# Kernel tuning notes

Hardware: AMD Instinct MI355X
Metric: run time of the kernel (lower is better)

Reference implementation:

```python
import jax, jax.numpy as jnp
import numpy as np

B, L, D_MODEL = 4, 2048, 512
N_HEAD, D_K, D_V = 8, 64, 64
RANK = 20


def tt_linear(x, g1, g2, g3, g4, b):
    # TT-matrix linear: input modes (4,4,8,4), output modes (4,4,8,4), ranks [1,20,20,20,1]
    Bx, Lx, _ = x.shape
    t = x.reshape(Bx * Lx, 4, 4, 8, 4)
    t = jnp.einsum('bwxyz,wou->bxyzou', t, g1[0])        # g1: [1,m1,n1,r1]
    t = jnp.einsum('bxyzou,uxpv->byzopv', t, g2)         # g2: [r1,m2,n2,r2]
    t = jnp.einsum('byzopv,vyqw->bzopqw', t, g3)         # g3: [r2,m3,n3,r3]
    t = jnp.einsum('bzopqw,wzs->bopqs', t, g4[..., 0])   # g4: [r3,m4,n4,1]
    return t.reshape(Bx, Lx, -1) + b


def setup_inputs() -> dict:
    key = jax.random.key(0)
    ks = jax.random.split(key, 8)
    scale = jnp.float32(0.15)
    inp = {}
    for name, kk in zip(['wq', 'wk', 'wv', 'fc'], ks[:4]):
        sub = jax.random.split(kk, 4)
        inp[name + '_g1'] = jax.random.normal(sub[0], (1, 4, 4, RANK), jnp.float32) * scale
        inp[name + '_g2'] = jax.random.normal(sub[1], (RANK, 4, 4, RANK), jnp.float32) * scale
        inp[name + '_g3'] = jax.random.normal(sub[2], (RANK, 8, 8, RANK), jnp.float32) * scale
        inp[name + '_g4'] = jax.random.normal(sub[3], (RANK, 4, 4, 1), jnp.float32) * scale
        inp[name + '_b'] = jnp.zeros((D_MODEL,), jnp.float32)
    inp['q'] = jax.random.normal(ks[4], (B, L, D_MODEL), jnp.float32)
    inp['k'] = jax.random.normal(ks[5], (B, L, D_MODEL), jnp.float32)
    inp['v'] = jax.random.normal(ks[6], (B, L, D_MODEL), jnp.float32)
    inp['ln_g'] = jnp.ones((D_MODEL,), jnp.float32)
    inp['ln_b'] = jnp.zeros((D_MODEL,), jnp.float32)
    return inp


def reference(q, k, v,
              wq_g1, wq_g2, wq_g3, wq_g4, wq_b,
              wk_g1, wk_g2, wk_g3, wk_g4, wk_b,
              wv_g1, wv_g2, wv_g3, wv_g4, wv_b,
              fc_g1, fc_g2, fc_g3, fc_g4, fc_b,
              ln_g, ln_b):
    Bx, Lq, _ = q.shape
    residual = q
    qh = tt_linear(q, wq_g1, wq_g2, wq_g3, wq_g4, wq_b).reshape(Bx, Lq, N_HEAD, D_K).transpose(0, 2, 1, 3)
    kh = tt_linear(k, wk_g1, wk_g2, wk_g3, wk_g4, wk_b).reshape(Bx, Lq, N_HEAD, D_K).transpose(0, 2, 1, 3)
    vh = tt_linear(v, wv_g1, wv_g2, wv_g3, wv_g4, wv_b).reshape(Bx, Lq, N_HEAD, D_V).transpose(0, 2, 1, 3)
    temp = jnp.sqrt(jnp.float32(D_K))
    attn = jnp.einsum('bhqd,bhkd->bhqk', qh / temp, kh)  # explicit [B,H,L,L] scores
    attn = jax.nn.softmax(attn, axis=-1)
    o = jnp.einsum('bhqk,bhkd->bhqd', attn, vh)
    o = o.transpose(0, 2, 1, 3).reshape(Bx, Lq, N_HEAD * D_V)
    out = tt_linear(o, fc_g1, fc_g2, fc_g3, fc_g4, fc_b) + residual
    mu = out.mean(-1, keepdims=True)
    var = out.var(-1, keepdims=True)
    out = (out - mu) / jnp.sqrt(var + 1e-12) * ln_g + ln_b
    return (out, attn)
```

## Files before the change

### kernel.cpp

```cpp
#include <hip/hip_runtime.h>
#include <hip/hip_bf16.h>
#include <math.h>

#define BB 4
#define LL 2048
#define DM 512
#define NH 8
#define DK 64
#define RANK 20

typedef __attribute__((ext_vector_type(8))) short short8;
typedef __attribute__((ext_vector_type(4))) short short4b;
typedef __attribute__((ext_vector_type(4))) float f32x4;
typedef __hip_bfloat16 bf16;

__device__ inline short to_bf(float x) {
    bf16 h = __float2bfloat16(x);
    return *reinterpret_cast<short*>(&h);
}

struct BwArgs {
    const float* g1[4]; const float* g2[4]; const float* g3[4]; const float* g4[4];
    bf16* wt[4];
};
__global__ __launch_bounds__(256) void build_w_kernel(BwArgs args)
{
    int s4 = blockIdx.y;
    const float* __restrict__ g1 = args.g1[s4];
    const float* __restrict__ g2 = args.g2[s4];
    const float* __restrict__ g3 = args.g3[s4];
    const float* __restrict__ g4 = args.g4[s4];
    bf16* __restrict__ Wt = args.wt[s4];

    int idx = blockIdx.x * 256 + threadIdx.x;
    if (idx >= 4*4*8*4*4*8) return;
    int q = idx & 7; int t = idx >> 3;
    int p = t & 3;  t >>= 2;
    int o = t & 3;  t >>= 2;
    int y = t & 7;  t >>= 3;
    int x = t & 3;  t >>= 2;
    int w = t & 3;

    float c[RANK];
    for (int v = 0; v < RANK; ++v) c[v] = 0.f;
    for (int u = 0; u < RANK; ++u) {
        float a = g1[(w*4 + o)*RANK + u];
        const float* g2p = g2 + ((u*4 + x)*4 + p)*RANK;
        for (int v = 0; v < RANK; ++v) c[v] += a * g2p[v];
    }
    float d[RANK];
    for (int r = 0; r < RANK; ++r) d[r] = 0.f;
    for (int v = 0; v < RANK; ++v) {
        float cv = c[v];
        const float* g3p = g3 + ((v*8 + y)*8 + q)*RANK;
        for (int r = 0; r < RANK; ++r) d[r] += cv * g3p[r];
    }
    for (int z = 0; z < 4; ++z) {
        for (int s = 0; s < 4; ++s) {
            float acc = 0.f;
            for (int r = 0; r < RANK; ++r) acc += d[r] * g4[(r*4 + z)*4 + s];
            int i = ((w*4 + x)*8 + y)*4 + z;
            int j = ((o*4 + p)*8 + q)*4 + s;
            Wt[(size_t)j*DM + i] = __float2bfloat16(acc);
        }
    }
}

struct CvtArgs { const float* src[3]; bf16* dst[3]; };
__global__ __launch_bounds__(256) void cvt_kernel(CvtArgs args)
{
    int a = blockIdx.y;
    const float* __restrict__ s = args.src[a];
    bf16* __restrict__ d = args.dst[a];
    size_t i = ((size_t)blockIdx.x * 256 + threadIdx.x) * 8;
    float4 v0 = *(const float4*)&s[i];
    float4 v1 = *(const float4*)&s[i + 4];
    short8 h;
    h[0] = to_bf(v0.x); h[1] = to_bf(v0.y); h[2] = to_bf(v0.z); h[3] = to_bf(v0.w);
    h[4] = to_bf(v1.x); h[5] = to_bf(v1.y); h[6] = to_bf(v1.z); h[7] = to_bf(v1.w);
    *(short8*)&d[i] = h;
}

#define GEMM_CORE64(Ap, Bp)                                                        \
    f32x4 acc[2][2] = {};                                                          \
    for (int k0 = 0; k0 < DM; k0 += 32) {                                          \
        short8 a[2], b[2];                                                         \
        _Pragma("unroll")                                                          \
        for (int mt = 0; mt < 2; ++mt)                                             \
            a[mt] = *(const short8*)&Ap[(size_t)(mt*16 + l15)*DM + k0 + l4*8];     \
        _Pragma("unroll")                                                          \
        for (int nt = 0; nt < 2; ++nt)                                             \
            b[nt] = *(const short8*)&Bp[(size_t)(nt*16 + l15)*DM + k0 + l4*8];     \
        _Pragma("unroll")                                                          \
        for (int mt = 0; mt < 2; ++mt)                                             \
            _Pragma("unroll")                                                      \
            for (int nt = 0; nt < 2; ++nt)                                         \
                acc[mt][nt] = __builtin_amdgcn_mfma_f32_16x16x32_bf16(             \
                    a[mt], b[nt], acc[mt][nt], 0, 0, 0);                           \
    }

struct QkvArgs {
    const bf16* A[3]; const bf16* W[3]; const float* bias[3];
    bf16* outQ; bf16* outK; bf16* outV;
};
__global__ __launch_bounds__(256) void gemm_qkv_kernel(QkvArgs args)
{
    int z = blockIdx.z;
    const bf16* __restrict__ A  = args.A[z];
    const bf16* __restrict__ Wt = args.W[z];
    const float* __restrict__ bias = args.bias[z];

    int m0 = blockIdx.x * 64, n0 = blockIdx.y * 64;
    int t = threadIdx.x, lane = t & 63, wave = t >> 6;
    int l15 = lane & 15, l4 = lane >> 4;
    int wm = wave >> 1, wn = wave & 1;
    const bf16* Ap = A  + (size_t)(m0 + wm*32)*DM;
    const bf16* Bp = Wt + (size_t)(n0 + wn*32)*DM;

    GEMM_CORE64(Ap, Bp)

    if (z < 2) {
        bf16* __restrict__ out = (z == 0) ? args.outQ : args.outK;
        float oscale = (z == 0) ? 0.18033688f : 1.0f;
        #pragma unroll
        for (int mt = 0; mt < 2; ++mt) {
            #pragma unroll
            for (int r = 0; r < 4; ++r) {
                int m = m0 + wm*32 + mt*16 + l4*4 + r;
                int l = m & (LL-1), bb = m >> 11;
                #pragma unroll
                for (int nt = 0; nt < 2; ++nt) {
                    int n = n0 + wn*32 + nt*16 + l15;
                    int h = n >> 6, d = n & 63;
                    float val = (acc[mt][nt][r] + bias[n]) * oscale;
                    out[(((size_t)(bb*NH + h))*LL + l)*DK + d] = __float2bfloat16(val);
                }
            }
        }
    } else {
        #pragma unroll
        for (int mt = 0; mt < 2; ++mt) {
            int mbase = m0 + wm*32 + mt*16 + l4*4;
            int l = mbase & (LL-1), bb = mbase >> 11;
            #pragma unroll
            for (int nt = 0; nt < 2; ++nt) {
                int n = n0 + wn*32 + nt*16 + l15;
                int h = n >> 6, d = n & 63;
                float bv = bias[n];
                short4b h4;
                #pragma unroll
                for (int r = 0; r < 4; ++r) h4[r] = to_bf(acc[mt][nt][r] + bv);
                *(short4b*)&args.outV[((size_t)(bb*NH + h)*DK + d)*LL + l] = h4;
            }
        }
    }
}

__global__ __launch_bounds__(256) void gemm_fc_kernel(
    const bf16* __restrict__ A, const bf16* __restrict__ Wt,
    const float* __restrict__ bias, float* __restrict__ out)
{
    int m0 = blockIdx.x * 64, n0 = blockIdx.y * 64;
    int t = threadIdx.x, lane = t & 63, wave = t >> 6;
    int l15 = lane & 15, l4 = lane >> 4;
    int wm = wave >> 1, wn = wave & 1;
    const bf16* Ap = A  + (size_t)(m0 + wm*32)*DM;
    const bf16* Bp = Wt + (size_t)(n0 + wn*32)*DM;

    GEMM_CORE64(Ap, Bp)

    #pragma unroll
    for (int mt = 0; mt < 2; ++mt) {
        #pragma unroll
        for (int r = 0; r < 4; ++r) {
            int m = m0 + wm*32 + mt*16 + l4*4 + r;
            #pragma unroll
            for (int nt = 0; nt < 2; ++nt) {
                int n = n0 + wn*32 + nt*16 + l15;
                out[(size_t)m*DM + n] = acc[mt][nt][r] + bias[n];
            }
        }
    }
}

__global__ __launch_bounds__(256, 4) void attn_kernel(
    const bf16* __restrict__ Qh, const bf16* __restrict__ Kh,
    const bf16* __restrict__ Vt, float* __restrict__ attn,
    bf16* __restrict__ O)
{
    __shared__ __align__(16) bf16 Ks[128][68];
    __shared__ __align__(16) bf16 Ps[4][16][152];

    int qt = blockIdx.x, bh = blockIdx.y;
    int q0 = qt * 64;
    int t = threadIdx.x, lane = t & 63, wave = t >> 6;
    int l15 = lane & 15, l4 = lane >> 4;
    int qr0 = wave * 16;

    const bf16* Qp = Qh + ((size_t)bh * LL + q0 + qr0) * DK;
    const bf16* Kp = Kh + (size_t)bh * LL * DK;
    const bf16* Vp = Vt + (size_t)bh * DK * LL;

    short8 aq0 = *(const short8*)&Qp[(size_t)l15*DK + l4*8];
    short8 aq1 = *(const short8*)&Qp[(size_t)l15*DK + 32 + l4*8];

    int srow = t >> 3, sseg = t & 7;

    float lsum[4] = {0.f, 0.f, 0.f, 0.f};
    f32x4 o_acc[4] = {};

    for (int kc = 0; kc < LL; kc += 128) {
        #pragma unroll
        for (int i = 0; i < 4; ++i) {
            int row = srow + i*32;
            *(short8*)&Ks[row][sseg*8] =
                *(const short8*)&Kp[(size_t)(kc + row)*DK + sseg*8];
        }
        __syncthreads();

        f32x4 s[8];
        #pragma unroll
        for (int ct = 0; ct < 8; ++ct) {
            short8 b0 = *(const short8*)&Ks[ct*16 + l15][l4*8];
            short8 b1 = *(const short8*)&Ks[ct*16 + l15][32 + l4*8];
            f32x4 acc = {0.f, 0.f, 0.f, 0.f};
            acc = __builtin_amdgcn_mfma_f32_16x16x32_bf16(aq0, b0, acc, 0, 0, 0);
            acc = __builtin_amdgcn_mfma_f32_16x16x32_bf16(aq1, b1, acc, 0, 0, 0);
            s[ct] = acc;
        }

        #pragma unroll
        for (int ct = 0; ct < 8; ++ct) {
            #pragma unroll
            for (int r = 0; r < 4; ++r) {
                float p = exp2f(s[ct][r]);
                lsum[r] += p;
                Ps[wave][l4*4 + r][ct*16 + l15] = __float2bfloat16(p);
            }
        }

        #pragma unroll
        for (int kt = 0; kt < 4; ++kt) {
            short8 a = *(const short8*)&Ps[wave][l15][kt*32 + l4*8];
            #pragma unroll
            for (int dt = 0; dt < 4; ++dt) {
                short8 b = *(const short8*)&Vp[(size_t)(dt*16 + l15)*LL + kc + kt*32 + l4*8];
                o_acc[dt] = __builtin_amdgcn_mfma_f32_16x16x32_bf16(a, b, o_acc[dt], 0, 0, 0);
            }
        }
        __syncthreads();
    }

    float invl[4];
    #pragma unroll
    for (int r = 0; r < 4; ++r) {
        float ss = lsum[r];
        #pragma unroll
        for (int off = 8; off >= 1; off >>= 1) ss += __shfl_xor(ss, off);
        invl[r] = 1.0f / ss;
    }

    {
        int bb = bh >> 3, h = bh & 7;
        #pragma unroll
        for (int dt = 0; dt < 4; ++dt)
            #pragma unroll
            for (int r = 0; r < 4; ++r) {
                int row = q0 + qr0 + l4*4 + r;
                O[((size_t)bb * LL + row) * DM + h*DK + dt*16 + l15] =
                    __float2bfloat16(o_acc[dt][r] * invl[r]);
            }
    }

    for (int kc = 0; kc < LL; kc += 128) {
        #pragma unroll
        for (int i = 0; i < 4; ++i) {
            int row = srow + i*32;
            *(short8*)&Ks[row][sseg*8] =
                *(const short8*)&Kp[(size_t)(kc + row)*DK + sseg*8];
        }
        __syncthreads();

        float* ap = attn + ((size_t)bh * LL + q0 + qr0) * LL + kc;
        #pragma unroll
        for (int ct = 0; ct < 8; ++ct) {
            short8 b0 = *(const short8*)&Ks[ct*16 + l15][l4*8];
            short8 b1 = *(const short8*)&Ks[ct*16 + l15][32 + l4*8];
            f32x4 s = {0.f, 0.f, 0.f, 0.f};
            s = __builtin_amdgcn_mfma_f32_16x16x32_bf16(aq0, b0, s, 0, 0, 0);
            s = __builtin_amdgcn_mfma_f32_16x16x32_bf16(aq1, b1, s, 0, 0, 0);
            #pragma unroll
            for (int r = 0; r < 4; ++r) {
                int row = l4*4 + r;
                ap[(size_t)row * LL + ct*16 + l15] = exp2f(s[r]) * invl[r];
            }
        }
        __syncthreads();
    }
}

__global__ __launch_bounds__(256) void ln_kernel(
    const float* __restrict__ Y, const float* __restrict__ Res,
    const float* __restrict__ g, const float* __restrict__ bta,
    float* __restrict__ out)
{
    int row = blockIdx.x;
    int t = threadIdx.x;
    const float* yp = Y  + (size_t)row*DM;
    const float* rp = Res + (size_t)row*DM;
    float v0 = yp[t]       + rp[t];
    float v1 = yp[t + 256] + rp[t + 256];
    float s1 = v0 + v1;
    float s2 = v0*v0 + v1*v1;
    __shared__ float red1[4], red2[4];
    #pragma unroll
    for (int off = 32; off >= 1; off >>= 1) {
        s1 += __shfl_xor(s1, off);
        s2 += __shfl_xor(s2, off);
    }
    int w = t >> 6;
    if ((t & 63) == 0) { red1[w] = s1; red2[w] = s2; }
    __syncthreads();
    float mu = (red1[0]+red1[1]+red1[2]+red1[3]) * (1.0f/DM);
    float ms = (red2[0]+red2[1]+red2[2]+red2[3]) * (1.0f/DM);
    float inv = rsqrtf(ms - mu*mu + 1e-12f);
    out[(size_t)row*DM + t]       = (v0 - mu)*inv*g[t]       + bta[t];
    out[(size_t)row*DM + t + 256] = (v1 - mu)*inv*g[t + 256] + bta[t + 256];
}

extern "C" void kernel_launch(void* const* d_in, const int* in_sizes, int n_in,
                              void* d_out, int out_size, void* d_ws, size_t ws_size,
                              hipStream_t stream)
{
    const float* G[4][5];
    for (int s = 0; s < 4; ++s)
        for (int i = 0; i < 5; ++i)
            G[s][i] = (const float*)d_in[s*5 + i];
    const float* q   = (const float*)d_in[20];
    const float* k   = (const float*)d_in[21];
    const float* v   = (const float*)d_in[22];
    const float* lng = (const float*)d_in[23];
    const float* lnb = (const float*)d_in[24];

    float* out  = (float*)d_out;
    float* attn = out + (size_t)BB*LL*DM;

    const size_t NTOK = (size_t)BB*LL*DM;
    bf16* wt  = (bf16*)d_ws;
    bf16* qbf = wt + 4*(size_t)DM*DM;
    bf16* kbf = qbf + NTOK;
    bf16* vbf = kbf + NTOK;
    bf16* qh  = vbf + NTOK;
    bf16* kh  = qh + NTOK;
    bf16* vt  = kh + NTOK;
    bf16* o   = vt + NTOK;
    float* y  = (float*)(o + NTOK);

    BwArgs bw;
    for (int s = 0; s < 4; ++s) {
        bw.g1[s] = G[s][0]; bw.g2[s] = G[s][1];
        bw.g3[s] = G[s][2]; bw.g4[s] = G[s][3];
        bw.wt[s] = wt + (size_t)s*DM*DM;
    }
    build_w_kernel<<<dim3(64, 4), 256, 0, stream>>>(bw);

    CvtArgs cv;
    cv.src[0] = q; cv.src[1] = k; cv.src[2] = v;
    cv.dst[0] = qbf; cv.dst[1] = kbf; cv.dst[2] = vbf;
    cvt_kernel<<<dim3(NTOK/(256*8), 3), 256, 0, stream>>>(cv);

    QkvArgs qa;
    qa.A[0] = qbf; qa.A[1] = kbf; qa.A[2] = vbf;
    qa.W[0] = wt; qa.W[1] = wt + (size_t)DM*DM; qa.W[2] = wt + 2*(size_t)DM*DM;
    qa.bias[0] = G[0][4]; qa.bias[1] = G[1][4]; qa.bias[2] = G[2][4];
    qa.outQ = qh; qa.outK = kh; qa.outV = vt;
    gemm_qkv_kernel<<<dim3(BB*LL/64, DM/64, 3), 256, 0, stream>>>(qa);

    attn_kernel<<<dim3(LL/64, BB*NH), 256, 0, stream>>>(qh, kh, vt, attn, o);

    gemm_fc_kernel<<<dim3(BB*LL/64, DM/64), 256, 0, stream>>>(
        o, wt + 3*(size_t)DM*DM, G[3][4], y);
    ln_kernel<<<BB*LL, 256, 0, stream>>>(y, q, lng, lnb, out);
}
```

Measured before the change: 426.6 us.

## Split attention into row-sum pre-pass and single fused probability/PV pass

```diff
diff --git a/kernel.cpp b/kernel.cpp
--- a/kernel.cpp
+++ b/kernel.cpp
@@ -183,10 +183,71 @@
     }
 }
 
-__global__ __launch_bounds__(256, 4) void attn_kernel(
+__global__ __launch_bounds__(256, 4) void attn_lsum_kernel(
     const bf16* __restrict__ Qh, const bf16* __restrict__ Kh,
-    const bf16* __restrict__ Vt, float* __restrict__ attn,
-    bf16* __restrict__ O)
+    float* __restrict__ invl_g)
+{
+    __shared__ float red[4][64];
+
+    int qt = blockIdx.x, bh = blockIdx.y;
+    int q0 = qt * 64;
+    int t = threadIdx.x, lane = t & 63, wave = t >> 6;
+    int l15 = lane & 15, l4 = lane >> 4;
+
+    const bf16* Qp = Qh + ((size_t)bh * LL + q0) * DK;
+    const bf16* Kp = Kh + ((size_t)bh * LL + wave * 512) * DK;
+
+    short8 aq[4][2];
+    #pragma unroll
+    for (int qs = 0; qs < 4; ++qs) {
+        aq[qs][0] = *(const short8*)&Qp[(size_t)(qs*16 + l15)*DK + l4*8];
+        aq[qs][1] = *(const short8*)&Qp[(size_t)(qs*16 + l15)*DK + 32 + l4*8];
+    }
+
+    float lsum[4][4] = {};
+    #pragma unroll 2
+    for (int kt = 0; kt < 32; ++kt) {
+        const bf16* kr = &Kp[(size_t)(kt*16 + l15)*DK + l4*8];
+        short8 b0 = *(const short8*)kr;
+        short8 b1 = *(const short8*)(kr + 32);
+        #pragma unroll
+        for (int qs = 0; qs < 4; ++qs) {
+            f32x4 s = {0.f, 0.f, 0.f, 0.f};
+            s = __builtin_amdgcn_mfma_f32_16x16x32_bf16(aq[qs][0], b0, s, 0, 0, 0);
+            s = __builtin_amdgcn_mfma_f32_16x16x32_bf16(aq[qs][1], b1, s, 0, 0, 0);
+            #pragma unroll
+            for (int r = 0; r < 4; ++r) lsum[qs][r] += exp2f(s[r]);
+        }
+    }
+
+    #pragma unroll
+    for (int qs = 0; qs < 4; ++qs)
+        #pragma unroll
+        for (int r = 0; r < 4; ++r) {
+            float v = lsum[qs][r];
+            #pragma unroll
+            for (int off = 8; off >= 1; off >>= 1) v += __shfl_xor(v, off);
+            lsum[qs][r] = v;
+        }
+
+    if (l15 == 0) {
+        #pragma unroll
+        for (int qs = 0; qs < 4; ++qs)
+            #pragma unroll
+            for (int r = 0; r < 4; ++r)
+                red[wave][qs*16 + l4*4 + r] = lsum[qs][r];
+    }
+    __syncthreads();
+    if (t < 64) {
+        float s = red[0][t] + red[1][t] + red[2][t] + red[3][t];
+        invl_g[(size_t)bh * LL + q0 + t] = 1.0f / s;
+    }
+}
+
+__global__ __launch_bounds__(256, 4) void attn_main_kernel(
+    const bf16* __restrict__ Qh, const bf16* __restrict__ Kh,
+    const bf16* __restrict__ Vt, const float* __restrict__ invl_g,
+    float* __restrict__ attn, bf16* __restrict__ O)
 {
     __shared__ __align__(16) bf16 Ks[128][68];
     __shared__ __align__(16) bf16 Ps[4][16][152];
@@ -204,11 +265,14 @@
     short8 aq0 = *(const short8*)&Qp[(size_t)l15*DK + l4*8];
     short8 aq1 = *(const short8*)&Qp[(size_t)l15*DK + 32 + l4*8];
 
+    float invl[4];
+    #pragma unroll
+    for (int r = 0; r < 4; ++r)
+        invl[r] = invl_g[(size_t)bh * LL + q0 + qr0 + l4*4 + r];
+
     int srow = t >> 3, sseg = t & 7;
 
-    float lsum[4] = {0.f, 0.f, 0.f, 0.f};
     f32x4 o_acc[4] = {};
-
     for (int kc = 0; kc < LL; kc += 128) {
         #pragma unroll
         for (int i = 0; i < 4; ++i) {
@@ -229,13 +293,15 @@
             s[ct] = acc;
         }
 
+        float* ap = attn + ((size_t)bh * LL + q0 + qr0) * LL + kc;
         #pragma unroll
         for (int ct = 0; ct < 8; ++ct) {
             #pragma unroll
             for (int r = 0; r < 4; ++r) {
-                float p = exp2f(s[ct][r]);
-                lsum[r] += p;
-                Ps[wave][l4*4 + r][ct*16 + l15] = __float2bfloat16(p);
+                int row = l4*4 + r;
+                float p = exp2f(s[ct][r]) * invl[r];
+                ap[(size_t)row * LL + ct*16 + l15] = p;
+                Ps[wave][row][ct*16 + l15] = __float2bfloat16(p);
             }
         }
 
@@ -251,52 +317,15 @@
         __syncthreads();
     }
 
-    float invl[4];
-    #pragma unroll
-    for (int r = 0; r < 4; ++r) {
-        float ss = lsum[r];
-        #pragma unroll
-        for (int off = 8; off >= 1; off >>= 1) ss += __shfl_xor(ss, off);
-        invl[r] = 1.0f / ss;
-    }
-
-    {
-        int bb = bh >> 3, h = bh & 7;
-        #pragma unroll
-        for (int dt = 0; dt < 4; ++dt)
-            #pragma unroll
-            for (int r = 0; r < 4; ++r) {
-                int row = q0 + qr0 + l4*4 + r;
-                O[((size_t)bb * LL + row) * DM + h*DK + dt*16 + l15] =
-                    __float2bfloat16(o_acc[dt][r] * invl[r]);
-            }
-    }
-
-    for (int kc = 0; kc < LL; kc += 128) {
-        #pragma unroll
-        for (int i = 0; i < 4; ++i) {
-            int row = srow + i*32;
-            *(short8*)&Ks[row][sseg*8] =
-                *(const short8*)&Kp[(size_t)(kc + row)*DK + sseg*8];
-        }
-        __syncthreads();
-
-        float* ap = attn + ((size_t)bh * LL + q0 + qr0) * LL + kc;
-        #pragma unroll
-        for (int ct = 0; ct < 8; ++ct) {
-            short8 b0 = *(const short8*)&Ks[ct*16 + l15][l4*8];
-            short8 b1 = *(const short8*)&Ks[ct*16 + l15][32 + l4*8];
-            f32x4 s = {0.f, 0.f, 0.f, 0.f};
-            s = __builtin_amdgcn_mfma_f32_16x16x32_bf16(aq0, b0, s, 0, 0, 0);
-            s = __builtin_amdgcn_mfma_f32_16x16x32_bf16(aq1, b1, s, 0, 0, 0);
-            #pragma unroll
-            for (int r = 0; r < 4; ++r) {
-                int row = l4*4 + r;
-                ap[(size_t)row * LL + ct*16 + l15] = exp2f(s[r]) * invl[r];
-            }
-        }
-        __syncthreads();
-    }
+    int bb = bh >> 3, h = bh & 7;
+    #pragma unroll
+    for (int dt = 0; dt < 4; ++dt)
+        #pragma unroll
+        for (int r = 0; r < 4; ++r) {
+            int row = q0 + qr0 + l4*4 + r;
+            O[((size_t)bb * LL + row) * DM + h*DK + dt*16 + l15] =
+                __float2bfloat16(o_acc[dt][r]);
+        }
 }
 
 __global__ __launch_bounds__(256) void ln_kernel(
@@ -355,6 +384,7 @@
     bf16* vt  = kh + NTOK;
     bf16* o   = vt + NTOK;
     float* y  = (float*)(o + NTOK);
+    float* invl = y + NTOK;
 
     BwArgs bw;
     for (int s = 0; s < 4; ++s) {
@@ -376,7 +406,8 @@
     qa.outQ = qh; qa.outK = kh; qa.outV = vt;
     gemm_qkv_kernel<<<dim3(BB*LL/64, DM/64, 3), 256, 0, stream>>>(qa);
 
-    attn_kernel<<<dim3(LL/64, BB*NH), 256, 0, stream>>>(qh, kh, vt, attn, o);
+    attn_lsum_kernel<<<dim3(LL/64, BB*NH), 256, 0, stream>>>(qh, kh, invl);
+    attn_main_kernel<<<dim3(LL/64, BB*NH), 256, 0, stream>>>(qh, kh, vt, invl, attn, o);
 
     gemm_fc_kernel<<<dim3(BB*LL/64, DM/64), 256, 0, stream>>>(
         o, wt + 3*(size_t)DM*DM, G[3][4], y);
```

New measurement: 556.2 us. 1.3x slower.
